# Kernel optimization log

Measured on AMD Instinct MI355X. Metric: run time of the kernel, lower is better.

Reference implementation:

```python
import jax, jax.numpy as jnp
import numpy as np

B, N, IN_DIM, D, H = 8, 2048, 256, 512, 4
HD = D // H
GX, GY = 8, 8
IMG_W, IMG_H = 256.0, 256.0
CW, CH = IMG_W / GX, IMG_H / GY
NBH = 1
EPS = 1e-5


def setup_inputs() -> dict:
    key = jax.random.key(0)
    ks = jax.random.split(key, 12)
    s = 0.02
    rn = lambda k, sh: jax.random.normal(k, sh, jnp.float32) * s
    return {
        'features': jax.random.normal(ks[0], (B, N, IN_DIM), jnp.float32),
        'coords': jax.random.uniform(ks[1], (B, N, 2), jnp.float32) * IMG_W,
        'W_feat': rn(ks[2], (IN_DIM, D)), 'b_feat': jnp.zeros((D,), jnp.float32),
        'W_p1': rn(ks[3], (2, D // 2)), 'b_p1': jnp.zeros((D // 2,), jnp.float32),
        'W_p2': rn(ks[4], (D // 2, D)), 'b_p2': jnp.zeros((D,), jnp.float32),
        'Wq': rn(ks[5], (D, D)), 'bq': jnp.zeros((D,), jnp.float32),
        'Wk': rn(ks[6], (D, D)), 'bk': jnp.zeros((D,), jnp.float32),
        'Wv': rn(ks[7], (D, D)), 'bv': jnp.zeros((D,), jnp.float32),
        'Wo': rn(ks[8], (D, D)), 'bo': jnp.zeros((D,), jnp.float32),
        'gamma': jnp.ones((D,), jnp.float32), 'beta': jnp.zeros((D,), jnp.float32),
    }


def reference(features, coords, W_feat, b_feat, W_p1, b_p1, W_p2, b_p2,
              Wq, bq, Wk, bk, Wv, bv, Wo, bo, gamma, beta):
    feat = features @ W_feat + b_feat                          # [B,N,D]
    # --- grid bucketing (mean feature per occupied cell) ---
    gx = jnp.clip((coords[..., 0] / CW).astype(jnp.int32), 0, GX - 1)
    gy = jnp.clip((coords[..., 1] / CH).astype(jnp.int32), 0, GY - 1)
    cell = gx * GY + gy                                        # [B,N]
    G = GX * GY
    seg = (jnp.arange(B, dtype=jnp.int32)[:, None] * G + cell).reshape(-1)
    sums = jax.ops.segment_sum(feat.reshape(B * N, D), seg, num_segments=B * G)
    counts = jax.ops.segment_sum(jnp.ones((B * N,), jnp.float32), seg, num_segments=B * G)
    mean = (sums / jnp.maximum(counts, 1.0)[:, None]).reshape(B, G, D)
    counts = counts.reshape(B, G)
    # --- neighbor cells (static 3x3 window for neighborhood=1) ---
    offs = np.array([(dx, dy) for dx in range(-NBH, NBH + 1) for dy in range(-NBH, NBH + 1)], np.int32)
    K = offs.shape[0]
    pe = jnp.asarray(offs, jnp.float32)
    pe = jax.nn.relu(pe @ W_p1 + b_p1) @ W_p2 + b_p2           # [K,D] pos enc of offsets
    ngx = gx[..., None] + offs[:, 0]                           # [B,N,K]
    ngy = gy[..., None] + offs[:, 1]
    inb = (ngx >= 0) & (ngx < GX) & (ngy >= 0) & (ngy < GY)
    nidx = jnp.clip(ngx, 0, GX - 1) * GY + jnp.clip(ngy, 0, GY - 1)
    bidx = jnp.arange(B)[:, None, None]
    valid = inb & (counts[bidx, nidx] > 0)                     # [B,N,K]
    keys = mean[bidx, nidx] + pe                               # [B,N,K,D]
    # --- per-point attention over <=9 neighbor cells ---
    q = (feat @ Wq + bq).reshape(B, N, H, HD)
    k = (keys @ Wk + bk).reshape(B, N, K, H, HD)
    v = (keys @ Wv + bv).reshape(B, N, K, H, HD)
    scores = jnp.einsum('bnhd,bnkhd->bnhk', q, k) / np.float32(np.sqrt(HD))
    scores = jnp.where(valid[:, :, None, :], scores, jnp.float32(-1e9))
    attn = jax.nn.softmax(scores, axis=-1)
    agg = jnp.einsum('bnhk,bnkhd->bnhd', attn, v).reshape(B, N, D) @ Wo + bo
    enhanced = feat + agg                                      # residual (dropout in eval = identity)
    mu = enhanced.mean(-1, keepdims=True)
    var = enhanced.var(-1, keepdims=True)
    return (enhanced - mu) / jnp.sqrt(var + EPS) * gamma + beta
```

## Files before the change

### kernel.cpp

```cpp
#include <hip/hip_runtime.h>
#include <stdint.h>

typedef unsigned short u16;
typedef unsigned int u32;
typedef __bf16 bf16x8 __attribute__((ext_vector_type(8)));
typedef float f32x4 __attribute__((ext_vector_type(4)));

#define NBATCH 8
#define NPT    2048
#define NPTS   16384
#define INDIM  256
#define DD     512
#define GG     64

__device__ __forceinline__ u16 f2bf(float f){
  u32 u = __builtin_bit_cast(u32, f);
  u += 0x7fffu + ((u >> 16) & 1u);
  return (u16)(u >> 16);
}
__device__ __forceinline__ float bf2f(u16 h){
  u32 u = ((u32)h) << 16;
  return __builtin_bit_cast(float, u);
}
__device__ __forceinline__ void load8(const float* __restrict__ p, float* r){
  float4 a = *(const float4*)p;
  float4 b = *(const float4*)(p + 4);
  r[0]=a.x;r[1]=a.y;r[2]=a.z;r[3]=a.w;r[4]=b.x;r[5]=b.y;r[6]=b.z;r[7]=b.w;
}
__device__ __forceinline__ void load8bf(const u16* __restrict__ p, float* r){
  uint4 v = *(const uint4*)p;
  r[0]=bf2f((u16)v.x); r[1]=bf2f((u16)(v.x>>16));
  r[2]=bf2f((u16)v.y); r[3]=bf2f((u16)(v.y>>16));
  r[4]=bf2f((u16)v.z); r[5]=bf2f((u16)(v.z>>16));
  r[6]=bf2f((u16)v.w); r[7]=bf2f((u16)(v.w>>16));
}
__device__ __forceinline__ void store8(float* __restrict__ p, const float* r){
  float4 a; a.x=r[0];a.y=r[1];a.z=r[2];a.w=r[3];
  float4 b; b.x=r[4];b.y=r[5];b.z=r[6];b.w=r[7];
  *(float4*)p = a; *(float4*)(p+4) = b;
}
__device__ __forceinline__ uint4 pack8(const float* a){
  uint4 pk;
  pk.x = (u32)f2bf(a[0]) | ((u32)f2bf(a[1]) << 16);
  pk.y = (u32)f2bf(a[2]) | ((u32)f2bf(a[3]) << 16);
  pk.z = (u32)f2bf(a[4]) | ((u32)f2bf(a[5]) << 16);
  pk.w = (u32)f2bf(a[6]) | ((u32)f2bf(a[7]) << 16);
  return pk;
}
typedef __attribute__((address_space(1))) unsigned as1u;
typedef __attribute__((address_space(3))) unsigned as3u;
__device__ __forceinline__ void gload16(const void* g, void* l){
  __builtin_amdgcn_global_load_lds((as1u*)(uintptr_t)g, (as3u*)(uintptr_t)l, 16, 0, 0);
}

__device__ __forceinline__ void transpose64(const float* __restrict__ src, int scols,
                                            u16* __restrict__ dst, int dcols,
                                            int r0, int c0, char* smem, int t){
  float (*sh)[65] = (float(*)[65])smem;
  #pragma unroll
  for (int i = 0; i < 16; i++){
    int idx = i*256 + t;
    int r = idx >> 6, c = idx & 63;
    sh[r][c] = src[(size_t)(r0 + r)*scols + c0 + c];
  }
  __syncthreads();
  #pragma unroll
  for (int i = 0; i < 8; i++){
    int idx = i*512 + t*2;
    int oR = idx >> 6, oC = idx & 63;
    u32 pk = (u32)f2bf(sh[oC][oR]) | ((u32)f2bf(sh[oC+1][oR]) << 16);
    *(u32*)(dst + (size_t)(c0 + oR)*dcols + r0 + oC) = pk;
  }
}

#define P_R1 2048
#define P_R2 2112
#define P_R3 2368
#define P_R4 2400
#define P_R5 2409
#define P_R6 2411
#define P_R7 2415
#define P_NB 2423
__global__ __launch_bounds__(256) void prep_kernel(
    const float* __restrict__ features, const float* __restrict__ W_feat,
    const float* __restrict__ Wq, const float* __restrict__ Wk,
    const float* __restrict__ Wv, const float* __restrict__ Wo,
    const float* __restrict__ W_p1, const float* __restrict__ b_p1,
    const float* __restrict__ W_p2, const float* __restrict__ b_p2,
    const float* __restrict__ b_feat, const float* __restrict__ bq,
    const float* __restrict__ bk, const float* __restrict__ bv,
    const float* __restrict__ coords,
    u16* __restrict__ featA, u16* __restrict__ W_feat_bf,
    u16* __restrict__ WqkvT, u16* __restrict__ WoT, u16* __restrict__ WcatT,
    u16* __restrict__ peD, float* __restrict__ bfq, float* __restrict__ biaskv,
    int* __restrict__ order, int* __restrict__ counts, int* __restrict__ cellstart)
{
  __shared__ __align__(16) char smem[34048];
  int bid = blockIdx.x, t = threadIdx.x;
  if (bid < P_R1){
    int i = bid*256 + t;
    float r[8]; load8(features + (size_t)i*8, r);
    *(uint4*)(featA + (size_t)i*8) = pack8(r);
  } else if (bid < P_R2){
    int i = (bid - P_R1)*256 + t;
    float r[8]; load8(W_feat + (size_t)i*8, r);
    *(uint4*)(W_feat_bf + (size_t)i*8) = pack8(r);
  } else if (bid < P_R3){
    int rel = bid - P_R2;
    int mat = rel >> 6, tile = rel & 63;
    int r0 = (tile >> 3)*64, c0 = (tile & 7)*64;
    const float* src = mat==0 ? Wq : (mat==1 ? Wk : (mat==2 ? Wv : Wo));
    u16* dst = mat==0 ? WqkvT : (mat==1 ? WqkvT + (size_t)512*DD
                     : (mat==2 ? WqkvT + (size_t)1024*DD : WoT));
    transpose64(src, DD, dst, DD, r0, c0, smem, t);
  } else if (bid < P_R4){
    int rel = bid - P_R3;
    int r0 = (rel >> 3)*64, c0 = (rel & 7)*64;
    transpose64(W_feat, DD, WcatT, INDIM, r0, c0, smem, t);
  } else if (bid < P_R5){
    int kk = bid - P_R4;
    float dx = (float)(kk/3 - 1), dy = (float)(kk%3 - 1);
    float* h = (float*)smem;
    float hv = dx*W_p1[t] + dy*W_p1[256 + t] + b_p1[t];
    h[t] = hv > 0.f ? hv : 0.f;
    __syncthreads();
    float acc0 = b_p2[t], acc1 = b_p2[t + 256];
    for (int c = 0; c < 256; c++){
      float hc = h[c];
      acc0 += hc * W_p2[(size_t)c*DD + t];
      acc1 += hc * W_p2[(size_t)c*DD + t + 256];
    }
    peD[(size_t)kk*DD + t]       = f2bf(acc0);
    peD[(size_t)kk*DD + t + 256] = f2bf(acc1);
  } else if (bid < P_R6){
    int i = (bid - P_R5)*256 + t;
    float* bfs = (float*)smem;
    bfs[t] = b_feat[t]; bfs[t + 256] = b_feat[t + 256];
    __syncthreads();
    float acc = 0.f;
    for (int k = 0; k < DD; k++) acc += bfs[k] * Wq[(size_t)k*DD + i];
    bfq[i] = acc + bq[i];
  } else if (bid < P_R7){
    int n = (bid - P_R6)*256 + t;
    float* bfs = (float*)smem;
    bfs[t] = b_feat[t]; bfs[t + 256] = b_feat[t + 256];
    __syncthreads();
    const float* W = (n < 512) ? Wk : Wv;
    int c = n & 511;
    float acc = 0.f;
    for (int k = 0; k < DD; k++) acc += bfs[k] * W[(size_t)k*DD + c];
    biaskv[n] = acc + ((n < 512) ? bk[c] : bv[c]);
  } else {
    int b = bid - P_R7;
    u16 (*hist)[65] = (u16(*)[65])smem;
    int* tot  = (int*)(smem + 33280);
    int* base = (int*)(smem + 33536);
    #pragma unroll
    for (int i = 0; i < 65; i++) hist[t][i] = 0;
    int myc[8];
    float cxy[16];
    load8(coords + (size_t)(b*NPT + t*8)*2,     cxy);
    load8(coords + (size_t)(b*NPT + t*8)*2 + 8, cxy + 8);
    #pragma unroll
    for (int i = 0; i < 8; i++){
      int gx = (int)(cxy[2*i]   * (1.0f/32.0f)); gx = gx < 0 ? 0 : (gx > 7 ? 7 : gx);
      int gy = (int)(cxy[2*i+1] * (1.0f/32.0f)); gy = gy < 0 ? 0 : (gy > 7 ? 7 : gy);
      myc[i] = gx*8 + gy;
      hist[t][myc[i]]++;
    }
    __syncthreads();
    if (t < GG){
      int acc = 0;
      for (int tt = 0; tt < 256; tt++){ int v = hist[tt][t]; hist[tt][t] = (u16)acc; acc += v; }
      tot[t] = acc;
    }
    __syncthreads();
    if (t == 0){
      int acc = 0;
      for (int g = 0; g < GG; g++){ base[g] = acc; acc += tot[g]; }
    }
    __syncthreads();
    if (t < GG){
      counts[b*GG + t] = tot[t];
      cellstart[b*GG + t] = base[t];
    }
    #pragma unroll
    for (int i = 0; i < 8; i++){
      int g = myc[i];
      int local = 0;
      #pragma unroll
      for (int j = 0; j < 8; j++) local += (j < i && myc[j] == g) ? 1 : 0;
      order[b*NPT + base[g] + (int)hist[t][g] + local] = t*8 + i;
    }
  }
}

#define BM 128
#define BN 128
#define GEMM_MAIN1D(Aptr, Btptr, Kv, GXv, NWGv, UIDX)                              \
  __shared__ __align__(16) u16 lA[BM*32];                                          \
  __shared__ __align__(16) u16 lB[BN*32];                                          \
  int tid = threadIdx.x;                                                           \
  int orig_ = (UIDX);                                                              \
  int swz_ = (orig_ & 7)*((NWGv) >> 3) + (orig_ >> 3);                             \
  int m0 = (swz_ / (GXv)) * BM, n0 = (swz_ % (GXv)) * BN;                          \
  int lane = tid & 63;                                                             \
  int wv = tid >> 6;                                                               \
  int wm = (wv >> 1) * 64, wn = (wv & 1) * 64;                                     \
  int lr = lane & 15;                                                              \
  int kg = (lane >> 4) << 3;                                                       \
  f32x4 acc[4][4] = {};                                                            \
  int srow = lane >> 2;                                                            \
  int scol = (lane & 3) << 3;                                                      \
  const u16* gA0 = (Aptr)  + (size_t)(m0 + wv*32 + srow)*(Kv) + scol;              \
  const u16* gB0 = (Btptr) + (size_t)(n0 + wv*32 + srow)*(Kv) + scol;              \
  u16* lA0 = lA + (wv*32)*32;                                                      \
  u16* lB0 = lB + (wv*32)*32;                                                      \
  for (int kt = 0; kt < (Kv); kt += 32){                                           \
    gload16(gA0 + kt,                   lA0);                                      \
    gload16(gA0 + kt + (size_t)16*(Kv), lA0 + 16*32);                              \
    gload16(gB0 + kt,                   lB0);                                      \
    gload16(gB0 + kt + (size_t)16*(Kv), lB0 + 16*32);                              \
    __syncthreads();                                                               \
    bf16x8 af[4], bfv[4];                                                          \
    _Pragma("unroll")                                                              \
    for (int i = 0; i < 4; i++) af[i]  = *(const bf16x8*)&lA[(wm + i*16 + lr)*32 + kg]; \
    _Pragma("unroll")                                                              \
    for (int j = 0; j < 4; j++) bfv[j] = *(const bf16x8*)&lB[(wn + j*16 + lr)*32 + kg]; \
    _Pragma("unroll")                                                              \
    for (int i = 0; i < 4; i++)                                                    \
      _Pragma("unroll")                                                            \
      for (int j = 0; j < 4; j++)                                                  \
        acc[i][j] = __builtin_amdgcn_mfma_f32_16x16x32_bf16(af[i], bfv[j], acc[i][j], 0, 0, 0); \
    __syncthreads();                                                               \
  }                                                                                \
  int lrow = (lane >> 4) << 2;

__global__ __launch_bounds__(256) void mid_kernel(
    const u16* __restrict__ WqkvT, const u16* __restrict__ W_feat_bf,
    const u16* __restrict__ peD, u16* __restrict__ Xout, float* __restrict__ meanKV,
    const u16* __restrict__ featA, const int* __restrict__ order,
    const int* __restrict__ counts, const int* __restrict__ cellstart,
    u16* __restrict__ meanF)
{
  if (blockIdx.x < 24){
    GEMM_MAIN1D(WqkvT, W_feat_bf, 512, 2, 24, (int)blockIdx.x)
    #pragma unroll
    for (int j = 0; j < 4; j++){
      int col = n0 + wn + j*16 + lr;
      #pragma unroll
      for (int i = 0; i < 4; i++){
        int row0 = m0 + wm + i*16 + lrow;
        #pragma unroll
        for (int r = 0; r < 4; r++)
          Xout[(size_t)(row0 + r)*INDIM + col] = f2bf(acc[i][j][r]);
      }
    }
  } else if (blockIdx.x < 60){
    __shared__ float pesh[512];
    int bid2 = blockIdx.x - 24;
    int kk = bid2 >> 2, seg = bid2 & 3;
    int t = threadIdx.x;
    int n = seg*256 + t;
    pesh[t]       = bf2f(peD[(size_t)kk*DD + t]);
    pesh[t + 256] = bf2f(peD[(size_t)kk*DD + t + 256]);
    __syncthreads();
    const u16* wrow = WqkvT + (size_t)(512 + n)*DD;
    float acc = 0.f;
    for (int d8 = 0; d8 < 64; d8++){
      float w8[8]; load8bf(wrow + d8*8, w8);
      #pragma unroll
      for (int j = 0; j < 8; j++) acc += pesh[d8*8 + j]*w8[j];
    }
    meanKV[(size_t)(512 + kk)*1024 + n] = acc;
  } else {
    __shared__ float part[128][2];
    int bg = blockIdx.x - 60;
    int b = bg >> 6;
    int t = threadIdx.x;
    int p = t & 127, half = t >> 7;
    int cnt = counts[bg], start = cellstart[bg];
    const int* ord = order + b*NPT + start;
    float a0 = 0.f, a1 = 0.f;
    for (int n = half; n < cnt; n += 2){
      u32 v = *(const u32*)(featA + (((size_t)(b*NPT + ord[n])) << 8) + p*2);
      a0 += bf2f((u16)v); a1 += bf2f((u16)(v >> 16));
    }
    if (half){ part[p][0] = a0; part[p][1] = a1; }
    __syncthreads();
    if (!half){
      a0 += part[p][0]; a1 += part[p][1];
      float inv = 1.f / (float)(cnt > 0 ? cnt : 1);
      *(u32*)(meanF + (size_t)bg*INDIM + p*2) =
          (u32)f2bf(a0*inv) | ((u32)f2bf(a1*inv) << 16);
    }
  }
}

__global__ __launch_bounds__(256) void featq_kernel(
    const u16* __restrict__ featA, const u16* __restrict__ WcatT,
    const u16* __restrict__ meanF, const u16* __restrict__ WfkvT,
    const float* __restrict__ bias0, const float* __restrict__ bias1,
    const float* __restrict__ biaskv,
    u16* __restrict__ feat_bf, u16* __restrict__ q_bf, float* __restrict__ meanKV)
{
  int isMean = blockIdx.x >= 1024;
  const u16* A  = isMean ? meanF : featA;
  const u16* Bt = isMean ? WfkvT : WcatT;
  int uidx = isMean ? ((int)blockIdx.x - 1024) : (int)blockIdx.x;
  int NWG  = isMean ? 32 : 1024;
  GEMM_MAIN1D(A, Bt, 256, 8, NWG, uidx)
  if (!isMean){
    int half = n0 >> 9;
    u16* outp = half ? q_bf : feat_bf;
    const float* bias = half ? bias1 : bias0;
    int nb = n0 & 511;
    #pragma unroll
    for (int j = 0; j < 4; j++){
      int col = nb + wn + j*16 + lr;
      float bcol = bias[col];
      #pragma unroll
      for (int i = 0; i < 4; i++){
        int row0 = m0 + wm + i*16 + lrow;
        #pragma unroll
        for (int r = 0; r < 4; r++)
          outp[(size_t)(row0 + r)*DD + col] = f2bf(acc[i][j][r] + bcol);
      }
    }
  } else {
    #pragma unroll
    for (int j = 0; j < 4; j++){
      int col = n0 + wn + j*16 + lr;
      float bcol = biaskv[col];
      #pragma unroll
      for (int i = 0; i < 4; i++){
        int row0 = m0 + wm + i*16 + lrow;
        #pragma unroll
        for (int r = 0; r < 4; r++)
          meanKV[(size_t)(row0 + r)*1024 + col] = acc[i][j][r] + bcol;
      }
    }
  }
}

__global__ __launch_bounds__(256) void lin_kernel(
    const u16* __restrict__ agg_bf, const u16* __restrict__ WoT,
    const float* __restrict__ bo, u16* __restrict__ lin_bf)
{
  GEMM_MAIN1D(agg_bf, WoT, 512, 4, 512, (int)blockIdx.x)
  #pragma unroll
  for (int j = 0; j < 4; j++){
    int col = n0 + wn + j*16 + lr;
    float bcol = bo[col];
    #pragma unroll
    for (int i = 0; i < 4; i++){
      int row0 = m0 + wm + i*16 + lrow;
      #pragma unroll
      for (int r = 0; r < 4; r++)
        lin_bf[(size_t)(row0 + r)*DD + col] = f2bf(acc[i][j][r] + bcol);
    }
  }
}

__global__ __launch_bounds__(256) void attn_cells(
    const u16* __restrict__ q, const float* __restrict__ meanKV,
    const int* __restrict__ order, const int* __restrict__ counts,
    const int* __restrict__ cellstart, u16* __restrict__ agg)
{
  int bg4 = blockIdx.x;
  int bg = bg4 >> 2, part = bg4 & 3;
  int b = bg >> 6, c = bg & 63;
  int gx = c >> 3, gy = c & 7;
  __shared__ __align__(16) u16 Kf[9][DD];
  __shared__ __align__(16) u16 Vf[9][DD];
  __shared__ int vrow[9];
  int t = threadIdx.x;
  if (t < 9){
    int dx = t/3 - 1, dy = t%3 - 1;
    int nx = gx + dx, ny = gy + dy;
    int inb = ((unsigned)nx < 8u) && ((unsigned)ny < 8u);
    int row = b*GG + (((nx&7) << 3) | (ny&7));
    vrow[t] = (inb && counts[row] > 0) ? row : -1;
  }
  __syncthreads();
  int d = 2*t;
  #pragma unroll
  for (int kk = 0; kk < 9; kk++){
    int row = vrow[kk];
    if (row >= 0){
      float2 mk = *(const float2*)&meanKV[(size_t)row*1024 + d];
      float2 pk = *(const float2*)&meanKV[(size_t)(512+kk)*1024 + d];
      float2 mv = *(const float2*)&meanKV[(size_t)row*1024 + 512 + d];
      float2 pv = *(const float2*)&meanKV[(size_t)(512+kk)*1024 + 512 + d];
      *(u32*)&Kf[kk][d] = (u32)f2bf(mk.x+pk.x) | ((u32)f2bf(mk.y+pk.y) << 16);
      *(u32*)&Vf[kk][d] = (u32)f2bf(mv.x+pv.x) | ((u32)f2bf(mv.y+pv.y) << 16);
    }
  }
  __syncthreads();
  int cnt = counts[bg];
  int wv = t >> 6, lane = t & 63;
  int widx = part*4 + wv;
  const int* ord = order + b*NPT + cellstart[bg];
  for (int i = widx; i < cnt; i += 16){
    size_t p = (size_t)b*NPT + ord[i];
    float qv[8];
    load8bf(q + p*DD + lane*8, qv);
    float s[9];
    #pragma unroll
    for (int kk = 0; kk < 9; kk++){
      float partial = 0.f;
      if (vrow[kk] >= 0){
        float kv[8]; load8bf(&Kf[kk][lane*8], kv);
        #pragma unroll
        for (int j = 0; j < 8; j++) partial += qv[j]*kv[j];
      }
      partial += __shfl_xor(partial, 1);
      partial += __shfl_xor(partial, 2);
      partial += __shfl_xor(partial, 4);
      partial += __shfl_xor(partial, 8);
      s[kk] = (vrow[kk] >= 0) ? partial * 0.08838834764831843f : -1e30f;
    }
    float mx = s[0];
    #pragma unroll
    for (int kk = 1; kk < 9; kk++) mx = fmaxf(mx, s[kk]);
    float w[9], sum = 0.f;
    #pragma unroll
    for (int kk = 0; kk < 9; kk++){
      w[kk] = (vrow[kk] >= 0) ? __expf(s[kk] - mx) : 0.f;
      sum += w[kk];
    }
    float inv = 1.f / sum;
    float a[8] = {0,0,0,0,0,0,0,0};
    #pragma unroll
    for (int kk = 0; kk < 9; kk++){
      if (vrow[kk] >= 0){
        float wk = w[kk] * inv;
        float vv[8]; load8bf(&Vf[kk][lane*8], vv);
        #pragma unroll
        for (int j = 0; j < 8; j++) a[j] += wk*vv[j];
      }
    }
    *(uint4*)&agg[p*DD + lane*8] = pack8(a);
  }
}

__global__ __launch_bounds__(256) void ln_kernel(
    const u16* __restrict__ feat, const u16* __restrict__ lin,
    const float* __restrict__ gamma, const float* __restrict__ beta,
    float* __restrict__ out)
{
  int wv = threadIdx.x >> 6, lane = threadIdx.x & 63;
  size_t r = (size_t)blockIdx.x * 4 + wv;
  int d0 = lane * 8;
  float fv[8], lv[8];
  load8bf(feat + r*DD + d0, fv);
  load8bf(lin  + r*DD + d0, lv);
  float e[8], s1 = 0.f, s2 = 0.f;
  #pragma unroll
  for (int j = 0; j < 8; j++){ e[j] = fv[j] + lv[j]; s1 += e[j]; s2 += e[j]*e[j]; }
  #pragma unroll
  for (int m = 1; m < 64; m <<= 1){ s1 += __shfl_xor(s1, m); s2 += __shfl_xor(s2, m); }
  float mu  = s1 * (1.f/512.f);
  float var = s2 * (1.f/512.f) - mu*mu;
  float istd = rsqrtf(var + 1e-5f);
  float gv[8], bev[8];
  load8(gamma + d0, gv); load8(beta + d0, bev);
  float o[8];
  #pragma unroll
  for (int j = 0; j < 8; j++) o[j] = (e[j] - mu)*istd*gv[j] + bev[j];
  store8(out + r*DD + d0, o);
}

extern "C" void kernel_launch(void* const* d_in, const int* in_sizes, int n_in,
                              void* d_out, int out_size, void* d_ws, size_t ws_size,
                              hipStream_t stream) {
  (void)in_sizes; (void)n_in; (void)out_size; (void)ws_size;
  const float* features = (const float*)d_in[0];
  const float* coords   = (const float*)d_in[1];
  const float* W_feat   = (const float*)d_in[2];
  const float* b_feat   = (const float*)d_in[3];
  const float* W_p1     = (const float*)d_in[4];
  const float* b_p1     = (const float*)d_in[5];
  const float* W_p2     = (const float*)d_in[6];
  const float* b_p2     = (const float*)d_in[7];
  const float* Wq = (const float*)d_in[8];  const float* bq = (const float*)d_in[9];
  const float* Wk = (const float*)d_in[10]; const float* bk = (const float*)d_in[11];
  const float* Wv = (const float*)d_in[12]; const float* bv = (const float*)d_in[13];
  const float* Wo = (const float*)d_in[14]; const float* bo = (const float*)d_in[15];
  const float* gamma = (const float*)d_in[16]; const float* beta = (const float*)d_in[17];
  float* out = (float*)d_out;

  char* ws = (char*)d_ws;
  size_t off = 0;
  auto alloc = [&](size_t bytes) -> void* {
    void* p = ws + off;
    off = (off + bytes + 255) & ~(size_t)255;
    return p;
  };
  u16*   featA     = (u16*)  alloc((size_t)NPTS*INDIM*2);
  u16*   feat_bf   = (u16*)  alloc((size_t)NPTS*DD*2);
  u16*   q_bf      = (u16*)  alloc((size_t)NPTS*DD*2);
  u16*   agg_bf    = (u16*)  alloc((size_t)NPTS*DD*2);
  u16*   lin_bf    = (u16*)  alloc((size_t)NPTS*DD*2);
  u16*   W_feat_bf = (u16*)  alloc((size_t)INDIM*DD*2);
  u16*   WqkvT     = (u16*)  alloc((size_t)1536*DD*2);
  u16*   WoT       = (u16*)  alloc((size_t)DD*DD*2);
  u16*   WcatT     = (u16*)  alloc((size_t)1024*INDIM*2);
  u16*   WfkvT     = (u16*)  alloc((size_t)1024*INDIM*2);
  u16*   peD       = (u16*)  alloc((size_t)9*DD*2);
  u16*   meanF     = (u16*)  alloc((size_t)512*INDIM*2);
  float* meanKV    = (float*)alloc((size_t)640*1024*4);
  float* bfq       = (float*)alloc((size_t)DD*4);
  float* biaskv    = (float*)alloc((size_t)1024*4);
  int*   order     = (int*)  alloc((size_t)NPTS*4);
  int*   counts    = (int*)  alloc((size_t)NBATCH*GG*4);
  int*   cellstart = (int*)  alloc((size_t)NBATCH*GG*4);
  u16*   Xout      = WcatT + (size_t)512*INDIM;

  prep_kernel<<<P_NB, 256, 0, stream>>>(
      features, W_feat, Wq, Wk, Wv, Wo, W_p1, b_p1, W_p2, b_p2,
      b_feat, bq, bk, bv, coords,
      featA, W_feat_bf, WqkvT, WoT, WcatT, peD, bfq, biaskv,
      order, counts, cellstart);
  mid_kernel<<<572, 256, 0, stream>>>(
      WqkvT, W_feat_bf, peD, Xout, meanKV, featA, order, counts, cellstart, meanF);
  featq_kernel<<<1056, 256, 0, stream>>>(
      featA, WcatT, meanF, WfkvT, b_feat, bfq, biaskv, feat_bf, q_bf, meanKV);
  attn_cells<<<NBATCH*GG*4, 256, 0, stream>>>(q_bf, meanKV, order, counts, cellstart, agg_bf);
  lin_kernel<<<512, 256, 0, stream>>>(agg_bf, WoT, bo, lin_bf);
  ln_kernel<<<NPTS/4, 256, 0, stream>>>(feat_bf, lin_bf, gamma, beta, out);
}
```

Before: 117.5 us.

## Double-buffer GEMM LDS tiles and merge attention cell blocks into one

The shared GEMM macro now double-buffers the A/B tiles in LDS and prefetches the next K-slice while MFMAs run on the current one. This removes one barrier per step and overlaps global loads with compute, at the cost of twice the LDS per block. The attention kernel goes from four 256-thread blocks per cell to one 1024-thread block. The 9-cell K/V staging is done once per cell instead of four times, which lowers occupancy flexibility and can leave tail imbalance.

```diff
diff --git a/kernel.cpp b/kernel.cpp
--- a/kernel.cpp
+++ b/kernel.cpp
@@ -197,9 +197,9 @@
 
 #define BM 128
 #define BN 128
-#define GEMM_MAIN1D(Aptr, Btptr, Kv, GXv, NWGv, UIDX)                              \
-  __shared__ __align__(16) u16 lA[BM*32];                                          \
-  __shared__ __align__(16) u16 lB[BN*32];                                          \
+#define GEMM_PIPE(Aptr, Btptr, Kv, GXv, NWGv, UIDX)                                \
+  __shared__ __align__(16) u16 lA[2][BM*32];                                       \
+  __shared__ __align__(16) u16 lB[2][BN*32];                                       \
   int tid = threadIdx.x;                                                           \
   int orig_ = (UIDX);                                                              \
   int swz_ = (orig_ & 7)*((NWGv) >> 3) + (orig_ >> 3);                             \
@@ -210,29 +210,39 @@
   int lr = lane & 15;                                                              \
   int kg = (lane >> 4) << 3;                                                       \
   f32x4 acc[4][4] = {};                                                            \
-  int srow = lane >> 2;                                                            \
-  int scol = (lane & 3) << 3;                                                      \
-  const u16* gA0 = (Aptr)  + (size_t)(m0 + wv*32 + srow)*(Kv) + scol;              \
-  const u16* gB0 = (Btptr) + (size_t)(n0 + wv*32 + srow)*(Kv) + scol;              \
-  u16* lA0 = lA + (wv*32)*32;                                                      \
-  u16* lB0 = lB + (wv*32)*32;                                                      \
-  for (int kt = 0; kt < (Kv); kt += 32){                                           \
-    gload16(gA0 + kt,                   lA0);                                      \
-    gload16(gA0 + kt + (size_t)16*(Kv), lA0 + 16*32);                              \
-    gload16(gB0 + kt,                   lB0);                                      \
-    gload16(gB0 + kt + (size_t)16*(Kv), lB0 + 16*32);                              \
+  {                                                                                \
+    int srow = lane >> 2;                                                          \
+    int scol = (lane & 3) << 3;                                                    \
+    const u16* gA0 = (Aptr)  + (size_t)(m0 + wv*32 + srow)*(Kv) + scol;            \
+    const u16* gB0 = (Btptr) + (size_t)(n0 + wv*32 + srow)*(Kv) + scol;            \
+    int lofs = (wv*32)*32;                                                         \
+    int steps = (Kv) >> 5;                                                         \
+    gload16(gA0,                   lA[0] + lofs);                                  \
+    gload16(gA0 + (size_t)16*(Kv), lA[0] + lofs + 16*32);                          \
+    gload16(gB0,                   lB[0] + lofs);                                  \
+    gload16(gB0 + (size_t)16*(Kv), lB[0] + lofs + 16*32);                          \
     __syncthreads();                                                               \
-    bf16x8 af[4], bfv[4];                                                          \
-    _Pragma("unroll")                                                              \
-    for (int i = 0; i < 4; i++) af[i]  = *(const bf16x8*)&lA[(wm + i*16 + lr)*32 + kg]; \
-    _Pragma("unroll")                                                              \
-    for (int j = 0; j < 4; j++) bfv[j] = *(const bf16x8*)&lB[(wn + j*16 + lr)*32 + kg]; \
-    _Pragma("unroll")                                                              \
-    for (int i = 0; i < 4; i++)                                                    \
+    for (int s = 0; s < steps; s++){                                               \
+      int cur = s & 1;                                                             \
+      if (s + 1 < steps){                                                          \
+        int kt = (s + 1) << 5;                                                     \
+        gload16(gA0 + kt,                   lA[cur^1] + lofs);                     \
+        gload16(gA0 + kt + (size_t)16*(Kv), lA[cur^1] + lofs + 16*32);             \
+        gload16(gB0 + kt,                   lB[cur^1] + lofs);                     \
+        gload16(gB0 + kt + (size_t)16*(Kv), lB[cur^1] + lofs + 16*32);             \
+      }                                                                            \
+      bf16x8 af[4], bfv[4];                                                        \
       _Pragma("unroll")                                                            \
-      for (int j = 0; j < 4; j++)                                                  \
-        acc[i][j] = __builtin_amdgcn_mfma_f32_16x16x32_bf16(af[i], bfv[j], acc[i][j], 0, 0, 0); \
-    __syncthreads();                                                               \
+      for (int i = 0; i < 4; i++) af[i]  = *(const bf16x8*)&lA[cur][(wm + i*16 + lr)*32 + kg]; \
+      _Pragma("unroll")                                                            \
+      for (int j = 0; j < 4; j++) bfv[j] = *(const bf16x8*)&lB[cur][(wn + j*16 + lr)*32 + kg]; \
+      _Pragma("unroll")                                                            \
+      for (int i = 0; i < 4; i++)                                                  \
+        _Pragma("unroll")                                                          \
+        for (int j = 0; j < 4; j++)                                                \
+          acc[i][j] = __builtin_amdgcn_mfma_f32_16x16x32_bf16(af[i], bfv[j], acc[i][j], 0, 0, 0); \
+      __syncthreads();                                                             \
+    }                                                                              \
   }                                                                                \
   int lrow = (lane >> 4) << 2;
 
@@ -244,7 +254,7 @@
     u16* __restrict__ meanF)
 {
   if (blockIdx.x < 24){
-    GEMM_MAIN1D(WqkvT, W_feat_bf, 512, 2, 24, (int)blockIdx.x)
+    GEMM_PIPE(WqkvT, W_feat_bf, 512, 2, 24, (int)blockIdx.x)
     #pragma unroll
     for (int j = 0; j < 4; j++){
       int col = n0 + wn + j*16 + lr;
@@ -309,7 +319,7 @@
   const u16* Bt = isMean ? WfkvT : WcatT;
   int uidx = isMean ? ((int)blockIdx.x - 1024) : (int)blockIdx.x;
   int NWG  = isMean ? 32 : 1024;
-  GEMM_MAIN1D(A, Bt, 256, 8, NWG, uidx)
+  GEMM_PIPE(A, Bt, 256, 8, NWG, uidx)
   if (!isMean){
     int half = n0 >> 9;
     u16* outp = half ? q_bf : feat_bf;
@@ -343,32 +353,12 @@
   }
 }
 
-__global__ __launch_bounds__(256) void lin_kernel(
-    const u16* __restrict__ agg_bf, const u16* __restrict__ WoT,
-    const float* __restrict__ bo, u16* __restrict__ lin_bf)
-{
-  GEMM_MAIN1D(agg_bf, WoT, 512, 4, 512, (int)blockIdx.x)
-  #pragma unroll
-  for (int j = 0; j < 4; j++){
-    int col = n0 + wn + j*16 + lr;
-    float bcol = bo[col];
-    #pragma unroll
-    for (int i = 0; i < 4; i++){
-      int row0 = m0 + wm + i*16 + lrow;
-      #pragma unroll
-      for (int r = 0; r < 4; r++)
-        lin_bf[(size_t)(row0 + r)*DD + col] = f2bf(acc[i][j][r] + bcol);
-    }
-  }
-}
-
-__global__ __launch_bounds__(256) void attn_cells(
+__global__ __launch_bounds__(1024) void attn_cells(
     const u16* __restrict__ q, const float* __restrict__ meanKV,
     const int* __restrict__ order, const int* __restrict__ counts,
     const int* __restrict__ cellstart, u16* __restrict__ agg)
 {
-  int bg4 = blockIdx.x;
-  int bg = bg4 >> 2, part = bg4 & 3;
+  int bg = blockIdx.x;
   int b = bg >> 6, c = bg & 63;
   int gx = c >> 3, gy = c & 7;
   __shared__ __align__(16) u16 Kf[9][DD];
@@ -383,9 +373,8 @@
     vrow[t] = (inb && counts[row] > 0) ? row : -1;
   }
   __syncthreads();
-  int d = 2*t;
-  #pragma unroll
-  for (int kk = 0; kk < 9; kk++){
+  int d = 2*(t & 255);
+  for (int kk = (t >> 8); kk < 9; kk += 4){
     int row = vrow[kk];
     if (row >= 0){
       float2 mk = *(const float2*)&meanKV[(size_t)row*1024 + d];
@@ -399,9 +388,8 @@
   __syncthreads();
   int cnt = counts[bg];
   int wv = t >> 6, lane = t & 63;
-  int widx = part*4 + wv;
   const int* ord = order + b*NPT + cellstart[bg];
-  for (int i = widx; i < cnt; i += 16){
+  for (int i = wv; i < cnt; i += 16){
     size_t p = (size_t)b*NPT + ord[i];
     float qv[8];
     load8bf(q + p*DD + lane*8, qv);
@@ -441,6 +429,25 @@
       }
     }
     *(uint4*)&agg[p*DD + lane*8] = pack8(a);
+  }
+}
+
+__global__ __launch_bounds__(256) void lin_kernel(
+    const u16* __restrict__ agg_bf, const u16* __restrict__ WoT,
+    const float* __restrict__ bo, u16* __restrict__ lin_bf)
+{
+  GEMM_PIPE(agg_bf, WoT, 512, 4, 512, (int)blockIdx.x)
+  #pragma unroll
+  for (int j = 0; j < 4; j++){
+    int col = n0 + wn + j*16 + lr;
+    float bcol = bo[col];
+    #pragma unroll
+    for (int i = 0; i < 4; i++){
+      int row0 = m0 + wm + i*16 + lrow;
+      #pragma unroll
+      for (int r = 0; r < 4; r++)
+        lin_bf[(size_t)(row0 + r)*DD + col] = f2bf(acc[i][j][r] + bcol);
+    }
   }
 }
 
@@ -526,7 +533,7 @@
       WqkvT, W_feat_bf, peD, Xout, meanKV, featA, order, counts, cellstart, meanF);
   featq_kernel<<<1056, 256, 0, stream>>>(
       featA, WcatT, meanF, WfkvT, b_feat, bfq, biaskv, feat_bf, q_bf, meanKV);
-  attn_cells<<<NBATCH*GG*4, 256, 0, stream>>>(q_bf, meanKV, order, counts, cellstart, agg_bf);
+  attn_cells<<<NBATCH*GG, 1024, 0, stream>>>(q_bf, meanKV, order, counts, cellstart, agg_bf);
   lin_kernel<<<512, 256, 0, stream>>>(agg_bf, WoT, bo, lin_bf);
   ln_kernel<<<NPTS/4, 256, 0, stream>>>(feat_bf, lin_bf, gamma, beta, out);
 }
```

Result: faster. 108.9 us (-7.3%).
